# Kernel tuning notes

Hardware: AMD Instinct MI355X
Metric: run time of the kernel (lower is better)

Reference implementation:

```python
import jax, jax.numpy as jnp
import numpy as np

N_NODES = 100000


def gcn_conv(x, W, b, row, col, ew, n_nodes):
    """PyG GCNConv: add self-loops (weight 1), symmetric normalization,
    out[c] = sum_{(r,c) in E} norm * (x @ W)[r] + b."""
    sl = jnp.arange(n_nodes, dtype=row.dtype)
    row2 = jnp.concatenate([row, sl])
    col2 = jnp.concatenate([col, sl])
    ew2 = jnp.concatenate([ew, jnp.ones((n_nodes,), dtype=ew.dtype)])
    deg = jax.ops.segment_sum(ew2, col2, num_segments=n_nodes)  # [N]
    dinv = jnp.where(deg > 0, jax.lax.rsqrt(jnp.where(deg > 0, deg, 1.0)), 0.0)
    norm = dinv[row2] * ew2 * dinv[col2]                         # [E+N]
    h = x @ W                                                    # [N, out]
    msg = h[row2] * norm[:, None]                                # gather + scale
    out = jax.ops.segment_sum(msg, col2, num_segments=n_nodes)   # scatter-add
    return out + b


def setup_inputs() -> dict:
    key = jax.random.key(0)
    k1, k2, k3, k4, k5 = jax.random.split(key, 5)
    F_IN, HID, C = 512, 16, 40
    E = 3200000
    x = jax.random.normal(k1, (N_NODES, F_IN), dtype=jnp.float32)
    edge_index = jax.random.randint(k2, (2, E), 0, N_NODES, dtype=jnp.int64)
    edge_weight = jax.random.uniform(k3, (E,), dtype=jnp.float32)
    # Glorot-ish init for weights
    W1 = jax.random.normal(k4, (F_IN, HID), dtype=jnp.float32) / np.sqrt(F_IN)
    b1 = jnp.zeros((HID,), dtype=jnp.float32)
    W2 = jax.random.normal(k5, (HID, C), dtype=jnp.float32) / np.sqrt(HID)
    b2 = jnp.zeros((C,), dtype=jnp.float32)
    return {"x": x, "edge_index": edge_index, "edge_weight": edge_weight,
            "W1": W1, "b1": b1, "W2": W2, "b2": b2}


def reference(x, edge_index, edge_weight, W1, b1, W2, b2):
    row, col = edge_index[0], edge_index[1]
    h = jax.nn.relu(gcn_conv(x, W1, b1, row, col, edge_weight, N_NODES))
    # dropout p=0.1 is identity at inference; DFALayer/DFA are identity in forward
    logits = gcn_conv(h, W2, b2, row, col, edge_weight, N_NODES)
    return jax.nn.log_softmax(logits, axis=1)
```

## Files before the change

### kernel.cpp

```cpp
#include <hip/hip_runtime.h>
#include <hip/hip_bf16.h>
#include <math.h>

#define F_IN 512
#define HID  16
#define C_OUT 40

#define BSH    7
#define BNODES 128
#define MAXNB  1024
#define CAP    5120

#define EPB 8192
#define CTH 512

__device__ __forceinline__ unsigned short f2bf(float f) {
    unsigned u = __float_as_uint(f);
    unsigned r = (u + 0x7FFF + ((u >> 16) & 1)) >> 16;
    return (unsigned short)r;
}
__device__ __forceinline__ float bf2f(unsigned short h) {
    return __uint_as_float(((unsigned)h) << 16);
}

__global__ __launch_bounds__(1024) void k_zero_arr(int* __restrict__ p, int n) {
    int i = blockIdx.x * 1024 + threadIdx.x;
    if (i < n) p[i] = 0;
}

__global__ __launch_bounds__(CTH) void k_part(const int* __restrict__ row,
                                              const int* __restrict__ col,
                                              const float* __restrict__ ew,
                                              int* __restrict__ bcnt,
                                              int* __restrict__ ncnt,
                                              int2* __restrict__ st,
                                              int E, int NB) {
    __shared__ int lc[MAXNB];
    __shared__ int lb[MAXNB];
    int t = threadIdx.x;
    for (int i = t; i < NB; i += CTH) lc[i] = 0;
    __syncthreads();
    int base = blockIdx.x * EPB;
#pragma unroll
    for (int i = 0; i < EPB / CTH; ++i) {
        int e = base + t + i * CTH;
        if (e < E) {
            int c = col[e];
            atomicAdd(&lc[c >> BSH], 1);
            atomicAdd(&ncnt[c], 1);
        }
    }
    __syncthreads();
    for (int i = t; i < NB; i += CTH) {
        int c = lc[i];
        lb[i] = c ? atomicAdd(&bcnt[i], c) : 0;
    }
    __syncthreads();
    for (int i = t; i < NB; i += CTH) lc[i] = 0;
    __syncthreads();
#pragma unroll
    for (int i = 0; i < EPB / CTH; ++i) {
        int e = base + t + i * CTH;
        if (e < E) {
            int c = col[e];
            int b = c >> BSH;
            int r = atomicAdd(&lc[b], 1);
            int idx = lb[b] + r;
            if (idx < CAP)
                st[(size_t)b * CAP + idx] =
                    make_int2((row[e] << BSH) | (c & (BNODES - 1)),
                              __float_as_int(ew[e]));
        }
    }
}

__global__ __launch_bounds__(512) void k_place(const int* __restrict__ bcnt,
                                               const int* __restrict__ ncnt,
                                               const int2* __restrict__ st,
                                               int2* __restrict__ st2,
                                               int2* __restrict__ noff,
                                               float* __restrict__ dinv, int N) {
    __shared__ int sc[BNODES];
    __shared__ int cl0[BNODES];
    __shared__ int rk[BNODES];
    __shared__ float ws[BNODES];
    int t = threadIdx.x, b = blockIdx.x;
    if (t < BNODES) {
        int n = b * BNODES + t;
        int c = (n < N) ? ncnt[n] : 0;
        cl0[t] = c; sc[t] = c; rk[t] = 0; ws[t] = 0.0f;
    }
    __syncthreads();
    for (int o = 1; o < BNODES; o <<= 1) {
        int v = (t < BNODES && t >= o) ? sc[t - o] : 0;
        __syncthreads();
        if (t < BNODES) sc[t] += v;
        __syncthreads();
    }
    int total = bcnt[b];
    if (total > CAP) total = CAP;
    size_t base = (size_t)b * CAP;
    for (int i = t; i < total; i += 512) {
        int2 rec = st[base + i];
        int cl = rec.x & (BNODES - 1);
        int r = atomicAdd(&rk[cl], 1);
        st2[base + (sc[cl] - cl0[cl]) + r] = make_int2(rec.x >> BSH, rec.y);
        atomicAdd(&ws[cl], __int_as_float(rec.y));
    }
    __syncthreads();
    if (t < BNODES) {
        int n = b * BNODES + t;
        if (n < N) {
            int bg = (int)base + sc[t] - cl0[t];
            noff[n] = make_int2(bg, bg + cl0[t]);
            dinv[n] = rsqrtf(1.0f + ws[t]);
        }
    }
}

#define ROWS_PER_WAVE 16

__global__ __launch_bounds__(256, 1) void k_gemm1(const float* __restrict__ x,
                                                  const float* __restrict__ W,
                                                  const float* __restrict__ dinv,
                                                  unsigned short* __restrict__ hb,
                                                  int N) {
    const int t = threadIdx.x;
    const int lane = t & 63;
    const int wv = blockIdx.x * 4 + (t >> 6);
    const int r0 = wv * ROWS_PER_WAVE;
    if (r0 >= N) return;
    const int rend = (r0 + ROWS_PER_WAVE < N) ? r0 + ROWS_PER_WAVE : N;

    float4 Wa[4][4], Wb[4][4];
    const float4* W4 = (const float4*)W;
#pragma unroll
    for (int q = 0; q < 4; ++q)
#pragma unroll
        for (int j4 = 0; j4 < 4; ++j4) {
            Wa[q][j4] = W4[(4 * lane + q) * 4 + j4];
            Wb[q][j4] = W4[(256 + 4 * lane + q) * 4 + j4];
        }

    const float4* xb4 = (const float4*)x;
    float4 pa = xb4[(size_t)r0 * 128 + lane];
    float4 pb = xb4[(size_t)r0 * 128 + 64 + lane];

    for (int r = r0; r < rend; ++r) {
        float4 ca = pa, cb = pb;
        if (r + 1 < rend) {
            pa = xb4[(size_t)(r + 1) * 128 + lane];
            pb = xb4[(size_t)(r + 1) * 128 + 64 + lane];
        }
        float acc[16];
#pragma unroll
        for (int j = 0; j < 16; ++j) acc[j] = 0.0f;
        const float xs0[4] = {ca.x, ca.y, ca.z, ca.w};
        const float xs1[4] = {cb.x, cb.y, cb.z, cb.w};
#pragma unroll
        for (int q = 0; q < 4; ++q) {
#pragma unroll
            for (int j4 = 0; j4 < 4; ++j4) {
                acc[j4 * 4 + 0] += xs0[q] * Wa[q][j4].x;
                acc[j4 * 4 + 1] += xs0[q] * Wa[q][j4].y;
                acc[j4 * 4 + 2] += xs0[q] * Wa[q][j4].z;
                acc[j4 * 4 + 3] += xs0[q] * Wa[q][j4].w;
            }
        }
#pragma unroll
        for (int q = 0; q < 4; ++q) {
#pragma unroll
            for (int j4 = 0; j4 < 4; ++j4) {
                acc[j4 * 4 + 0] += xs1[q] * Wb[q][j4].x;
                acc[j4 * 4 + 1] += xs1[q] * Wb[q][j4].y;
                acc[j4 * 4 + 2] += xs1[q] * Wb[q][j4].z;
                acc[j4 * 4 + 3] += xs1[q] * Wb[q][j4].w;
            }
        }

        const int b0 = lane & 1;
        float v8[8];
#pragma unroll
        for (int m = 0; m < 8; ++m) {
            float lo = acc[m], hi = acc[m + 8];
            float sent = b0 ? lo : hi;
            float recv = __shfl_xor(sent, 1, 64);
            float keep = b0 ? hi : lo;
            v8[m] = keep + recv;
        }
        const int b1 = (lane >> 1) & 1;
        float v4[4];
#pragma unroll
        for (int m = 0; m < 4; ++m) {
            float lo = v8[m], hi = v8[m + 4];
            float sent = b1 ? lo : hi;
            float recv = __shfl_xor(sent, 2, 64);
            float keep = b1 ? hi : lo;
            v4[m] = keep + recv;
        }
        const int b2 = (lane >> 2) & 1;
        float v2[2];
#pragma unroll
        for (int m = 0; m < 2; ++m) {
            float lo = v4[m], hi = v4[m + 2];
            float sent = b2 ? lo : hi;
            float recv = __shfl_xor(sent, 4, 64);
            float keep = b2 ? hi : lo;
            v2[m] = keep + recv;
        }
        const int b3 = (lane >> 3) & 1;
        float v1;
        {
            float lo = v2[0], hi = v2[1];
            float sent = b3 ? lo : hi;
            float recv = __shfl_xor(sent, 8, 64);
            float keep = b3 ? hi : lo;
            v1 = keep + recv;
        }
        v1 += __shfl_xor(v1, 16, 64);
        v1 += __shfl_xor(v1, 32, 64);

        float d = dinv[r];
        if (lane < 16) {
            int j = ((lane & 1) << 3) | (((lane >> 1) & 1) << 2) |
                    (((lane >> 2) & 1) << 1) | ((lane >> 3) & 1);
            hb[(size_t)r * HID + j] = f2bf(d * v1);
        }
    }
}

__global__ __launch_bounds__(256) void k_agg1(const int2* __restrict__ noff,
                                              const float* __restrict__ dinv,
                                              const int2* __restrict__ st2,
                                              const unsigned short* __restrict__ srcb,
                                              const float* __restrict__ bias,
                                              unsigned short* __restrict__ dstb,
                                              int N) {
    int t = threadIdx.x;
    int lane = t & 63, w = t >> 6;
    int n = blockIdx.x * 4 + w;
    if (n >= N) return;
    int q = lane & 3, i = lane >> 2;
    int2 be = noff[n];
    int beg = be.x, end = be.y;
    float4 acc = make_float4(0.f, 0.f, 0.f, 0.f);
    for (int e = beg + i; e < end; e += 16) {
        int2 rec = st2[e];
        float wt = __int_as_float(rec.y);
        ushort4 v = ((const ushort4*)(srcb + (size_t)rec.x * HID))[q];
        acc.x += wt * bf2f(v.x);
        acc.y += wt * bf2f(v.y);
        acc.z += wt * bf2f(v.z);
        acc.w += wt * bf2f(v.w);
    }
#pragma unroll
    for (int off = 4; off < 64; off <<= 1) {
        acc.x += __shfl_xor(acc.x, off, 64);
        acc.y += __shfl_xor(acc.y, off, 64);
        acc.z += __shfl_xor(acc.z, off, 64);
        acc.w += __shfl_xor(acc.w, off, 64);
    }
    if (i == 0) {
        float d = dinv[n];
        ushort4 sv = ((const ushort4*)(srcb + (size_t)n * HID))[q];
        float4 bq = ((const float4*)bias)[q];
        float r0 = d * fmaxf(d * (acc.x + bf2f(sv.x)) + bq.x, 0.f);
        float r1 = d * fmaxf(d * (acc.y + bf2f(sv.y)) + bq.y, 0.f);
        float r2 = d * fmaxf(d * (acc.z + bf2f(sv.z)) + bq.z, 0.f);
        float r3 = d * fmaxf(d * (acc.w + bf2f(sv.w)) + bq.w, 0.f);
        ((ushort4*)(dstb + (size_t)n * HID))[q] =
            make_ushort4(f2bf(r0), f2bf(r1), f2bf(r2), f2bf(r3));
    }
}

__global__ __launch_bounds__(256) void k_agg2(const int2* __restrict__ noff,
                                              const float* __restrict__ dinv,
                                              const int2* __restrict__ st2,
                                              const unsigned short* __restrict__ srcb,
                                              const float* __restrict__ W2,
                                              const float* __restrict__ b2,
                                              float* __restrict__ out, int N) {
    __shared__ float Ws[HID * C_OUT];
    __shared__ float bs[C_OUT];
    int t = threadIdx.x;
    for (int iw = t; iw < HID * C_OUT; iw += 256) Ws[iw] = W2[iw];
    if (t < C_OUT) bs[t] = b2[t];
    __syncthreads();

    int lane = t & 63, w = t >> 6;
    int n = blockIdx.x * 4 + w;
    if (n >= N) return;
    int q = lane & 3, i = lane >> 2;
    int2 be = noff[n];
    int beg = be.x, end = be.y;
    float4 acc = make_float4(0.f, 0.f, 0.f, 0.f);
    for (int e = beg + i; e < end; e += 16) {
        int2 rec = st2[e];
        float wt = __int_as_float(rec.y);
        ushort4 v = ((const ushort4*)(srcb + (size_t)rec.x * HID))[q];
        acc.x += wt * bf2f(v.x);
        acc.y += wt * bf2f(v.y);
        acc.z += wt * bf2f(v.z);
        acc.w += wt * bf2f(v.w);
    }
#pragma unroll
    for (int off = 4; off < 64; off <<= 1) {
        acc.x += __shfl_xor(acc.x, off, 64);
        acc.y += __shfl_xor(acc.y, off, 64);
        acc.z += __shfl_xor(acc.z, off, 64);
        acc.w += __shfl_xor(acc.w, off, 64);
    }
    float d = dinv[n];
    ushort4 sv = ((const ushort4*)(srcb + (size_t)n * HID))[q];
    float gq[4];
    gq[0] = d * (acc.x + bf2f(sv.x));
    gq[1] = d * (acc.y + bf2f(sv.y));
    gq[2] = d * (acc.z + bf2f(sv.z));
    gq[3] = d * (acc.w + bf2f(sv.w));
    float g16[16];
    int base = lane & ~3;
#pragma unroll
    for (int qq = 0; qq < 4; ++qq) {
#pragma unroll
        for (int k = 0; k < 4; ++k)
            g16[qq * 4 + k] = __shfl(gq[k], base + qq, 64);
    }
    float logit = -INFINITY;
    if (lane < C_OUT) {
        float a = bs[lane];
#pragma unroll
        for (int j = 0; j < HID; ++j) a += g16[j] * Ws[j * C_OUT + lane];
        logit = a;
    }
    float m = logit;
#pragma unroll
    for (int off = 32; off > 0; off >>= 1) m = fmaxf(m, __shfl_xor(m, off, 64));
    float ex = (lane < C_OUT) ? __expf(logit - m) : 0.0f;
    float s = ex;
#pragma unroll
    for (int off = 32; off > 0; off >>= 1) s += __shfl_xor(s, off, 64);
    if (lane < C_OUT) out[(size_t)n * C_OUT + lane] = logit - m - __logf(s);
}

extern "C" void kernel_launch(void* const* d_in, const int* in_sizes, int n_in,
                              void* d_out, int out_size, void* d_ws, size_t ws_size,
                              hipStream_t stream) {
    const float* x   = (const float*)d_in[0];
    const int*   ei  = (const int*)d_in[1];
    const float* ew  = (const float*)d_in[2];
    const float* W1  = (const float*)d_in[3];
    const float* b1  = (const float*)d_in[4];
    const float* W2  = (const float*)d_in[5];
    const float* b2  = (const float*)d_in[6];
    float* out = (float*)d_out;

    const int N = in_sizes[0] / F_IN;
    const int E = in_sizes[2];
    const int* row = ei;
    const int* col = ei + E;
    const int NB = (N + BNODES - 1) >> BSH;

    int* wsi = (int*)d_ws;
    size_t o = 0;
    int* ncnt  = wsi + o; o += N;
    int* bcnt  = wsi + o; o += MAXNB;
    int2* noff = (int2*)(wsi + o); o += (size_t)2 * N;
    float* dinv = (float*)(wsi + o); o += N;
    unsigned short* h1b = (unsigned short*)(wsi + o); o += (size_t)N * HID / 2;
    unsigned short* a1b = (unsigned short*)(wsi + o); o += (size_t)N * HID / 2;
    int2* st   = (int2*)(wsi + o); o += (size_t)NB * CAP * 2;
    int2* st2  = (int2*)(wsi + o); o += (size_t)NB * CAP * 2;

    int gZ = (N + MAXNB + 1023) / 1024;
    int gC = (E + EPB - 1) / EPB;
    int gW = (N + 3) / 4;
    int gG = (N + 4 * ROWS_PER_WAVE - 1) / (4 * ROWS_PER_WAVE);

    k_zero_arr<<<gZ, 1024, 0, stream>>>(ncnt, N + MAXNB);
    k_part<<<gC, CTH, 0, stream>>>(row, col, ew, bcnt, ncnt, st, E, NB);
    k_place<<<NB, 512, 0, stream>>>(bcnt, ncnt, st, st2, noff, dinv, N);
    k_gemm1<<<gG, 256, 0, stream>>>(x, W1, dinv, h1b, N);
    k_agg1<<<gW, 256, 0, stream>>>(noff, dinv, st2, h1b, b1, a1b, N);
    k_agg2<<<gW, 256, 0, stream>>>(noff, dinv, st2, a1b, W2, b2, out, N);
}
```

Before: 650.3 us.

## Stage partitioned edges in LDS and drop global per-node atomic counters

```diff
diff --git a/kernel.cpp b/kernel.cpp
--- a/kernel.cpp
+++ b/kernel.cpp
@@ -9,9 +9,10 @@
 #define BSH    7
 #define BNODES 128
 #define MAXNB  1024
+#define NBK    784
 #define CAP    5120
 
-#define EPB 8192
+#define EPB 4096
 #define CTH 512
 
 __device__ __forceinline__ unsigned short f2bf(float f) {
@@ -23,40 +24,53 @@
     return __uint_as_float(((unsigned)h) << 16);
 }
 
-__global__ __launch_bounds__(1024) void k_zero_arr(int* __restrict__ p, int n) {
-    int i = blockIdx.x * 1024 + threadIdx.x;
-    if (i < n) p[i] = 0;
+__global__ __launch_bounds__(1024) void k_zero(int* __restrict__ g, int n) {
+    int t = threadIdx.x;
+    if (t < n) g[t] = 0;
 }
 
 __global__ __launch_bounds__(CTH) void k_part(const int* __restrict__ row,
                                               const int* __restrict__ col,
                                               const float* __restrict__ ew,
                                               int* __restrict__ bcnt,
-                                              int* __restrict__ ncnt,
                                               int2* __restrict__ st,
                                               int E, int NB) {
-    __shared__ int lc[MAXNB];
-    __shared__ int lb[MAXNB];
+    __shared__ int2 lsort[EPB];
+    __shared__ int  dstL[EPB];
+    __shared__ int  lc[NBK];
+    __shared__ int  sb[NBK];
+    __shared__ int  lb[NBK];
+    __shared__ int  rk[NBK];
     int t = threadIdx.x;
-    for (int i = t; i < NB; i += CTH) lc[i] = 0;
+    for (int i = t; i < NBK; i += CTH) lc[i] = 0;
     __syncthreads();
     int base = blockIdx.x * EPB;
 #pragma unroll
     for (int i = 0; i < EPB / CTH; ++i) {
         int e = base + t + i * CTH;
-        if (e < E) {
-            int c = col[e];
-            atomicAdd(&lc[c >> BSH], 1);
-            atomicAdd(&ncnt[c], 1);
-        }
+        if (e < E) atomicAdd(&lc[col[e] >> BSH], 1);
     }
     __syncthreads();
     for (int i = t; i < NB; i += CTH) {
         int c = lc[i];
         lb[i] = c ? atomicAdd(&bcnt[i], c) : 0;
-    }
-    __syncthreads();
-    for (int i = t; i < NB; i += CTH) lc[i] = 0;
+        rk[i] = 0;
+    }
+    if (t < 64) {
+        int run = 0;
+        for (int c0 = 0; c0 < NB; c0 += 64) {
+            int i = c0 + t;
+            int v = (i < NB) ? lc[i] : 0;
+            int s = v;
+#pragma unroll
+            for (int off = 1; off < 64; off <<= 1) {
+                int u = __shfl_up(s, off, 64);
+                if (t >= off) s += u;
+            }
+            if (i < NB) sb[i] = run + s - v;
+            run += __shfl(s, 63, 64);
+        }
+    }
     __syncthreads();
 #pragma unroll
     for (int i = 0; i < EPB / CTH; ++i) {
@@ -64,57 +78,69 @@
         if (e < E) {
             int c = col[e];
             int b = c >> BSH;
-            int r = atomicAdd(&lc[b], 1);
-            int idx = lb[b] + r;
-            if (idx < CAP)
-                st[(size_t)b * CAP + idx] =
-                    make_int2((row[e] << BSH) | (c & (BNODES - 1)),
-                              __float_as_int(ew[e]));
-        }
-    }
-}
-
-__global__ __launch_bounds__(512) void k_place(const int* __restrict__ bcnt,
-                                               const int* __restrict__ ncnt,
-                                               const int2* __restrict__ st,
-                                               int2* __restrict__ st2,
-                                               int2* __restrict__ noff,
-                                               float* __restrict__ dinv, int N) {
-    __shared__ int sc[BNODES];
-    __shared__ int cl0[BNODES];
-    __shared__ int rk[BNODES];
-    __shared__ float ws[BNODES];
-    int t = threadIdx.x, b = blockIdx.x;
-    if (t < BNODES) {
-        int n = b * BNODES + t;
-        int c = (n < N) ? ncnt[n] : 0;
-        cl0[t] = c; sc[t] = c; rk[t] = 0; ws[t] = 0.0f;
-    }
-    __syncthreads();
-    for (int o = 1; o < BNODES; o <<= 1) {
-        int v = (t < BNODES && t >= o) ? sc[t - o] : 0;
-        __syncthreads();
-        if (t < BNODES) sc[t] += v;
-        __syncthreads();
-    }
+            int r = atomicAdd(&rk[b], 1);
+            int pos = sb[b] + r;
+            lsort[pos] = make_int2((row[e] << BSH) | (c & (BNODES - 1)),
+                                   __float_as_int(ew[e]));
+            int gi = lb[b] + r;
+            dstL[pos] = (gi < CAP) ? (b * CAP + gi) : -1;
+        }
+    }
+    __syncthreads();
+    int total = (base + EPB <= E) ? EPB : (E - base);
+    for (int i = t; i < total; i += CTH) {
+        int d = dstL[i];
+        if (d >= 0) st[d] = lsort[i];
+    }
+}
+
+__global__ __launch_bounds__(512) void k_sort(const int* __restrict__ bcnt,
+                                              const int2* __restrict__ st,
+                                              int2* __restrict__ st2,
+                                              int2* __restrict__ noff,
+                                              float* __restrict__ dinv, int N) {
+    __shared__ int cnt[BNODES];
+    __shared__ float wsum[BNODES];
+    __shared__ int off[BNODES];
+    int t = threadIdx.x;
+    int b = blockIdx.x;
+    if (t < BNODES) { cnt[t] = 0; wsum[t] = 0.0f; }
+    __syncthreads();
     int total = bcnt[b];
     if (total > CAP) total = CAP;
     size_t base = (size_t)b * CAP;
-    for (int i = t; i < total; i += 512) {
-        int2 rec = st[base + i];
+    for (int e = t; e < total; e += 512) {
+        int2 rec = st[base + e];
         int cl = rec.x & (BNODES - 1);
-        int r = atomicAdd(&rk[cl], 1);
-        st2[base + (sc[cl] - cl0[cl]) + r] = make_int2(rec.x >> BSH, rec.y);
-        atomicAdd(&ws[cl], __int_as_float(rec.y));
-    }
-    __syncthreads();
+        atomicAdd(&cnt[cl], 1);
+        atomicAdd(&wsum[cl], __int_as_float(rec.y));
+    }
+    __syncthreads();
+    if (t < BNODES) off[t] = cnt[t];
+    __syncthreads();
+    for (int o = 1; o < BNODES; o <<= 1) {
+        int v = (t < BNODES && t >= o) ? off[t - o] : 0;
+        __syncthreads();
+        if (t < BNODES) off[t] += v;
+        __syncthreads();
+    }
     if (t < BNODES) {
+        int ex = off[t] - cnt[t];
+        off[t] = ex;
         int n = b * BNODES + t;
         if (n < N) {
-            int bg = (int)base + sc[t] - cl0[t];
-            noff[n] = make_int2(bg, bg + cl0[t]);
-            dinv[n] = rsqrtf(1.0f + ws[t]);
-        }
+            int bg = (int)base + ex;
+            noff[n] = make_int2(bg, bg + cnt[t]);
+            dinv[n] = rsqrtf(1.0f + wsum[t]);
+        }
+        cnt[t] = 0;
+    }
+    __syncthreads();
+    for (int e = t; e < total; e += 512) {
+        int2 rec = st[base + e];
+        int cl = rec.x & (BNODES - 1);
+        int r = atomicAdd(&cnt[cl], 1);
+        st2[base + off[cl] + r] = make_int2(rec.x >> BSH, rec.y);
     }
 }
 
@@ -362,7 +388,6 @@
 
     int* wsi = (int*)d_ws;
     size_t o = 0;
-    int* ncnt  = wsi + o; o += N;
     int* bcnt  = wsi + o; o += MAXNB;
     int2* noff = (int2*)(wsi + o); o += (size_t)2 * N;
     float* dinv = (float*)(wsi + o); o += N;
@@ -371,14 +396,13 @@
     int2* st   = (int2*)(wsi + o); o += (size_t)NB * CAP * 2;
     int2* st2  = (int2*)(wsi + o); o += (size_t)NB * CAP * 2;
 
-    int gZ = (N + MAXNB + 1023) / 1024;
     int gC = (E + EPB - 1) / EPB;
     int gW = (N + 3) / 4;
     int gG = (N + 4 * ROWS_PER_WAVE - 1) / (4 * ROWS_PER_WAVE);
 
-    k_zero_arr<<<gZ, 1024, 0, stream>>>(ncnt, N + MAXNB);
-    k_part<<<gC, CTH, 0, stream>>>(row, col, ew, bcnt, ncnt, st, E, NB);
-    k_place<<<NB, 512, 0, stream>>>(bcnt, ncnt, st, st2, noff, dinv, N);
+    k_zero<<<1, 1024, 0, stream>>>(bcnt, NB);
+    k_part<<<gC, CTH, 0, stream>>>(row, col, ew, bcnt, st, E, NB);
+    k_sort<<<NB, 512, 0, stream>>>(bcnt, st, st2, noff, dinv, N);
     k_gemm1<<<gG, 256, 0, stream>>>(x, W1, dinv, h1b, N);
     k_agg1<<<gW, 256, 0, stream>>>(noff, dinv, st2, h1b, b1, a1b, N);
     k_agg2<<<gW, 256, 0, stream>>>(noff, dinv, st2, a1b, W2, b2, out, N);
```

Result: faster. 543.8 us (-16.4%).
